# Kernel optimization log

Measured on AMD Instinct MI355X. Metric: run time of the kernel, lower is better.

Reference implementation:

```python
import jax, jax.numpy as jnp
from jax import lax
import numpy as np

T, B, H, L = 512, 64, 512, 2


def _ran_layer(x, c0, w_ih, w_hh, b, length):
    """x: [T,B,H], c0: [B,H]; returns (output [T,B,H], c_T [B,H])."""
    wi = jnp.einsum('tbi,ih->tbh', x, w_ih)  # precompute input projections

    def step(c, inp):
        t, x_t, wi_t = inp
        g = c @ w_hh + b + wi_t                      # [B, 2H]
        f, i = jnp.split(g, 2, axis=1)
        c1 = jax.nn.sigmoid(i) * x_t + jax.nn.sigmoid(f) * jnp.tanh(c)
        mask = (t < length)[:, None].astype(c1.dtype)  # length-mask blend
        c1 = c1 * mask + c * (1.0 - mask)
        return c1, c1

    ts = jnp.arange(x.shape[0])
    cT, out = lax.scan(step, c0, (ts, x, wi))
    return out, cT


def setup_inputs() -> dict:
    key = jax.random.key(0)
    ks = jax.random.split(key, 8)
    stdv = 1.0 / np.sqrt(H)

    def u(k, shape):
        return jax.random.uniform(k, shape, jnp.float32, -stdv, stdv)

    return {
        'input_': jax.random.normal(ks[0], (T, B, H), jnp.float32),
        'hx': jnp.zeros((L, B, H), jnp.float32),
        'length': jax.random.randint(ks[1], (B,), 0, T, jnp.int64 if jax.config.jax_enable_x64 else jnp.int32),
        'w_ih_0': u(ks[2], (H, 2 * H)),
        'w_hh_0': u(ks[3], (H, 2 * H)),
        'b_0': jnp.zeros((2 * H,), jnp.float32),
        'w_ih_1': u(ks[4], (H, 2 * H)),
        'w_hh_1': u(ks[5], (H, 2 * H)),
        'b_1': jnp.zeros((2 * H,), jnp.float32),
    }


def reference(input_, hx, length, w_ih_0, w_hh_0, b_0, w_ih_1, w_hh_1, b_1):
    params = [(w_ih_0, w_hh_0, b_0), (w_ih_1, w_hh_1, b_1)]
    x = input_
    c_n = []
    for layer in range(L):
        w_ih, w_hh, b = params[layer]
        x, cT = _ran_layer(x, hx[layer], w_ih, w_hh, b, length)
        c_n.append(cT)
    return x, jnp.stack(c_n, 0)
```

## Files before the change

kernel.cpp:

```cpp
#include <hip/hip_runtime.h>

#define T_ 512
#define B_ 64
#define H_ 512
#define G_ 1024

typedef _Float16 f16;
typedef _Float16 h2 __attribute__((ext_vector_type(2)));
typedef _Float16 h4 __attribute__((ext_vector_type(4)));
typedef _Float16 f16x8 __attribute__((ext_vector_type(8)));
typedef float f32x4 __attribute__((ext_vector_type(4)));
typedef unsigned long long u64;

#define SPINMAX (1 << 22)

__device__ __forceinline__ float dot8_h(uint4 w, uint4 c, float acc) {
    union U { uint4 u; h2 h[4]; };
    U uw; uw.u = w;
    U uc; uc.u = c;
#if defined(__has_builtin) && __has_builtin(__builtin_amdgcn_fdot2)
    acc = __builtin_amdgcn_fdot2(uw.h[0], uc.h[0], acc, false);
    acc = __builtin_amdgcn_fdot2(uw.h[1], uc.h[1], acc, false);
    acc = __builtin_amdgcn_fdot2(uw.h[2], uc.h[2], acc, false);
    acc = __builtin_amdgcn_fdot2(uw.h[3], uc.h[3], acc, false);
#else
#pragma unroll
    for (int i = 0; i < 4; ++i) {
        acc += (float)uw.h[i][0] * (float)uc.h[i][0];
        acc += (float)uw.h[i][1] * (float)uc.h[i][1];
    }
#endif
    return acc;
}

__device__ __forceinline__ float sigm(float x) { return 1.f / (1.f + __expf(-x)); }

__device__ __forceinline__ u64 ldA64(const u64* p) {
    return __hip_atomic_load(p, __ATOMIC_RELAXED, __HIP_MEMORY_SCOPE_AGENT);
}
__device__ __forceinline__ void stA32(unsigned* p, unsigned v) {
    __hip_atomic_store(p, v, __ATOMIC_RELAXED, __HIP_MEMORY_SCOPE_AGENT);
}

__global__ void pack_fp16(const float* __restrict__ src, uint4* __restrict__ dst) {
    int idx = blockIdx.x * 256 + threadIdx.x;
    int j  = idx & (G_ - 1);
    int k8 = idx >> 10;
    union U { uint4 u; f16 h[8]; } v;
#pragma unroll
    for (int i = 0; i < 8; ++i)
        v.h[i] = (f16)src[(size_t)(k8 * 8 + i) * G_ + j];
    dst[idx] = v.u;
}

__global__ void pack_wcols(const float* __restrict__ src, uint4* __restrict__ dst) {
    int idx = blockIdx.x * 256 + threadIdx.x;
    int col = idx & 1023, k2 = idx >> 10;
    union U { uint4 u; f16 h[8]; } v;
#pragma unroll
    for (int i = 0; i < 8; ++i)
        v.h[i] = (f16)src[(size_t)(k2 * 8 + i) * G_ + col];
    dst[(size_t)col * 64 + k2] = v.u;
}

__global__ void pack_wT(const float* __restrict__ w, f16* __restrict__ bt) {
    int idx = blockIdx.x * 256 + threadIdx.x;
    int k = idx & 511, n = idx >> 9;
    bt[idx] = (f16)w[(size_t)k * G_ + n];
}

__launch_bounds__(256, 2)
__global__ void mfma_gemm_axf32(const float* __restrict__ A, const f16* __restrict__ BT,
                                const float* __restrict__ bias, f16* __restrict__ C) {
    __shared__ __align__(16) f16 aLds[128][64 + 8];
    __shared__ __align__(16) f16 bLds[128][64 + 8];
    const int tid = threadIdx.x;
    const int bm = blockIdx.x, bn = blockIdx.y;
    const int lane = tid & 63, wid = tid >> 6;
    const int wm = wid & 1, wn = wid >> 1;
    const int fr = lane & 15, fg = lane >> 4;

    f32x4 acc[4][4] = {};

    for (int kt = 0; kt < 8; ++kt) {
#pragma unroll
        for (int p = 0; p < 8; ++p) {
            int i = p * 256 + tid;
            int row = i >> 4, kc = (i & 15) * 4;
            float4 av = *(const float4*)&A[((size_t)(bm * 128 + row)) * 512 + kt * 64 + kc];
            h4 hv = {(f16)av.x, (f16)av.y, (f16)av.z, (f16)av.w};
            *(h4*)&aLds[row][kc] = hv;
        }
#pragma unroll
        for (int p = 0; p < 4; ++p) {
            int i = p * 256 + tid;
            int row = i >> 3, slot = i & 7;
            uint4 bv = *(const uint4*)&BT[((size_t)(bn * 128 + row)) * 512 + kt * 64 + slot * 8];
            *(uint4*)&bLds[row][slot * 8] = bv;
        }
        __syncthreads();
#pragma unroll
        for (int kf = 0; kf < 2; ++kf) {
            const int k0 = kf * 32 + fg * 8;
            f16x8 af[4], bf[4];
#pragma unroll
            for (int mi = 0; mi < 4; ++mi)
                af[mi] = *(const f16x8*)&aLds[wm * 64 + mi * 16 + fr][k0];
#pragma unroll
            for (int ni = 0; ni < 4; ++ni)
                bf[ni] = *(const f16x8*)&bLds[wn * 64 + ni * 16 + fr][k0];
#pragma unroll
            for (int mi = 0; mi < 4; ++mi)
#pragma unroll
                for (int ni = 0; ni < 4; ++ni)
                    acc[mi][ni] = __builtin_amdgcn_mfma_f32_16x16x32_f16(
                        af[mi], bf[ni], acc[mi][ni], 0, 0, 0);
        }
        __syncthreads();
    }

#pragma unroll
    for (int mi = 0; mi < 4; ++mi) {
#pragma unroll
        for (int ni = 0; ni < 4; ++ni) {
            int n = bn * 128 + wn * 64 + ni * 16 + fr;
            float bv = bias[n];
#pragma unroll
            for (int r = 0; r < 4; ++r) {
                int m = bm * 128 + wm * 64 + mi * 16 + fg * 4 + r;
                C[(size_t)m * G_ + n] = (f16)(acc[mi][ni][r] + bv);
            }
        }
    }
}

#define GM 128
#define GN 64
#define GK 16
__launch_bounds__(256)
__global__ void gemm_bias_f16(const float* __restrict__ A,
                              const float* __restrict__ Bm,
                              const float* __restrict__ bias,
                              f16* __restrict__ C, int M) {
    __shared__ __align__(16) float Als[GK][GM + 4];
    __shared__ __align__(16) float Bls[GK][GN];
    int tid = threadIdx.x;
    int m_base = blockIdx.x * GM;
    int n_base = blockIdx.y * GN;
    int tx = tid & 15, ty = tid >> 4;
    int m0 = ty * 8, n0 = tx * 4;
    float acc[8][4] = {};

    for (int k0 = 0; k0 < H_; k0 += GK) {
#pragma unroll
        for (int r = 0; r < 2; ++r) {
            int idx2 = tid + 256 * r;
            int row = idx2 >> 2, kc = (idx2 & 3) * 4;
            float4 av = *(const float4*)&A[(size_t)(m_base + row) * H_ + k0 + kc];
            Als[kc + 0][row] = av.x;
            Als[kc + 1][row] = av.y;
            Als[kc + 2][row] = av.z;
            Als[kc + 3][row] = av.w;
        }
        {
            int kk = tid >> 4, colb = (tid & 15) * 4;
            float4 bv = *(const float4*)&Bm[(size_t)(k0 + kk) * G_ + n_base + colb];
            *(float4*)&Bls[kk][colb] = bv;
        }
        __syncthreads();
#pragma unroll
        for (int kk = 0; kk < GK; ++kk) {
            float a0[8], b0[4];
            *(float4*)&a0[0] = *(const float4*)&Als[kk][m0];
            *(float4*)&a0[4] = *(const float4*)&Als[kk][m0 + 4];
            *(float4*)&b0[0] = *(const float4*)&Bls[kk][n0];
#pragma unroll
            for (int im = 0; im < 8; ++im)
#pragma unroll
                for (int in = 0; in < 4; ++in)
                    acc[im][in] += a0[im] * b0[in];
        }
        __syncthreads();
    }
    float bv[4];
    *(float4*)&bv[0] = *(const float4*)&bias[n_base + n0];
#pragma unroll
    for (int im = 0; im < 8; ++im) {
        h4 hv;
#pragma unroll
        for (int in = 0; in < 4; ++in) hv[in] = (f16)(acc[im][in] + bv[in]);
        *(h4*)&C[(size_t)(m_base + m0 + im) * G_ + n_base + n0] = hv;
    }
}

template <int PATH>
__launch_bounds__(1024, 1)
__global__ void ran_scan(const float* __restrict__ x_in, float* __restrict__ x_out,
                         float* __restrict__ c_out, const float* __restrict__ c0,
                         const int* __restrict__ length,
                         const uint4* __restrict__ whh_p,
                         const f16* __restrict__ wi, const float* __restrict__ bias,
                         const float* __restrict__ whh_f, const float* __restrict__ wih_f) {
    __shared__ __align__(16) f16 c_h[H_];
    __shared__ __align__(16) float c_f32[H_];
    __shared__ __align__(16) float x_f32[H_];
    __shared__ float g_i_lds[H_];

    const int b = blockIdx.x, tid = threadIdx.x;
    int len = length[b];
    if (len < 0) len = 0;
    if (len > T_) len = T_;

    float c1 = 0.f;
    if (tid < H_) {
        c1 = c0[(size_t)b * H_ + tid];
        c_h[tid] = (f16)c1;
        if (PATH == 2) c_f32[tid] = c1;
    }
    const float bj = (PATH == 0) ? 0.f : bias[tid];
    __syncthreads();

    for (int t = 0; t < len; ++t) {
        const size_t base = ((size_t)t * B_ + b) * H_;
        float xv = 0.f;
        if (tid < H_) {
            xv = x_in[base + tid];
            if (PATH == 2) x_f32[tid] = xv;
        }
        if (PATH == 2) __syncthreads();

        float g;
        if (PATH == 0) g = (float)wi[((size_t)t * B_ + b) * G_ + tid];
        else           g = bj;

        if (PATH == 0) {
            const uint4* cc = (const uint4*)c_h;
#pragma unroll 4
            for (int k8 = 0; k8 < H_ / 8; ++k8)
                g = dot8_h(whh_p[(size_t)k8 * G_ + tid], cc[k8], g);
        } else {
#pragma unroll 2
            for (int k = 0; k < H_; k += 4) {
                float4 cv = *(const float4*)&c_f32[k];
                g += cv.x * whh_f[(size_t)(k + 0) * G_ + tid];
                g += cv.y * whh_f[(size_t)(k + 1) * G_ + tid];
                g += cv.z * whh_f[(size_t)(k + 2) * G_ + tid];
                g += cv.w * whh_f[(size_t)(k + 3) * G_ + tid];
            }
#pragma unroll 2
            for (int k = 0; k < H_; k += 4) {
                float4 xvv = *(const float4*)&x_f32[k];
                g += xvv.x * wih_f[(size_t)(k + 0) * G_ + tid];
                g += xvv.y * wih_f[(size_t)(k + 1) * G_ + tid];
                g += xvv.z * wih_f[(size_t)(k + 2) * G_ + tid];
                g += xvv.w * wih_f[(size_t)(k + 3) * G_ + tid];
            }
        }

        if (tid >= H_) g_i_lds[tid - H_] = g;
        __syncthreads();
        if (tid < H_) {
            float gi = g_i_lds[tid];
            float c_old = c1;
            c1 = sigm(gi) * xv + sigm(g) * tanhf(c_old);
            c_h[tid] = (f16)c1;
            if (PATH == 2) c_f32[tid] = c1;
            x_out[base + tid] = c1;
        }
        __syncthreads();
    }

    if (tid < H_) {
        for (int t = len; t < T_; ++t)
            x_out[((size_t)t * B_ + b) * H_ + tid] = c1;
        c_out[(size_t)b * H_ + tid] = c1;
    }
}

__global__ __launch_bounds__(1024, 1)
void scan_mfma16(const float* __restrict__ x_in, const f16* __restrict__ wi,
                 const uint4* __restrict__ wpack, const float* __restrict__ c0,
                 const int* __restrict__ length, float* __restrict__ out,
                 float* __restrict__ cn, unsigned* __restrict__ cbuf,
                 int base_tag) {
    __shared__ __align__(16) f16 c_h[2][H_];
    __shared__ __align__(16) float2 g_part[2][128];
    __shared__ float c_fin[2][64];

    const int tid = threadIdx.x;
    const int bg = blockIdx.x & 31, s = blockIdx.x >> 5;
    const int b0 = bg * 2;
    const int w = tid >> 6, lane = tid & 63;
    const int n16 = lane & 15, kg = lane >> 4;
    const int p_grp = w >> 1, h = w & 1;

    const int gc = p_grp * 16 + n16;
    const int gcol = (gc < 64) ? (s * 64 + gc) : (512 + s * 64 + (gc - 64));
    uint4 wreg[8];
    {
        const uint4* wp = wpack + (size_t)gcol * 64 + kg;
#pragma unroll
        for (int k = 0; k < 8; ++k) wreg[k] = wp[(h * 8 + k) * 4];
    }

    if (tid < H_) {
        c_h[0][tid] = (f16)c0[(size_t)b0 * H_ + tid];
        c_h[1][tid] = (f16)c0[(size_t)(b0 + 1) * H_ + tid];
    }
    int len0 = length[b0], len1 = length[b0 + 1];
    len0 = min(max(len0, 0), T_);
    len1 = min(max(len1, 0), T_);
    const int maxlen = max(len0, len1);

    const int ab = (n16 < 2) ? n16 : 1;
    const int fb = tid >> 6, fcol = tid & 63;
    const int jj = s * 64 + fcol;
    const int myb = b0 + fb;
    const int mylen = fb ? len1 : len0;
    float c_old = 0.f;
    if (tid < 128) c_old = c0[(size_t)myb * H_ + jj];
    __syncthreads();

    for (int t = 0; t < maxlen; ++t) {
        float xv = 0.f, wif = 0.f, wii = 0.f;
        if (tid < 128) {
            size_t rb = (size_t)t * B_ + myb;
            xv  = x_in[rb * H_ + jj];
            wif = (float)wi[rb * G_ + jj];
            wii = (float)wi[rb * G_ + 512 + jj];
        }

        {
            f32x4 acc = {};
#pragma unroll
            for (int k = 0; k < 8; ++k) {
                const int m = h * 8 + k;
                f16x8 af = *(const f16x8*)&c_h[ab][m * 32 + kg * 8];
                acc = __builtin_amdgcn_mfma_f32_16x16x32_f16(
                    af, *(const f16x8*)&wreg[k], acc, 0, 0, 0);
            }
            if (lane < 16)
                g_part[h][p_grp * 16 + lane] = make_float2(acc[0], acc[1]);
        }
        __syncthreads();

        const int p1 = (t + 1) & 1;
        const unsigned tagw = (unsigned)(base_tag + t + 1) & 0xffffu;

        if (tid < 128) {
            float2 vf0 = g_part[0][fcol],      vf1 = g_part[1][fcol];
            float2 vi0 = g_part[0][64 + fcol], vi1 = g_part[1][64 + fcol];
            float gf = (fb ? (vf0.y + vf1.y) : (vf0.x + vf1.x)) + wif;
            float gi = (fb ? (vi0.y + vi1.y) : (vi0.x + vi1.x)) + wii;
            float c1;
            if (t < mylen) {
                float e2 = __expf(2.f * c_old);
                float th = (e2 - 1.f) / (e2 + 1.f);
                c1 = sigm(gi) * xv + sigm(gf) * th;
            } else {
                c1 = c_old;
            }
            c_old = c1;
            union { f16 h2u; unsigned short u; } cv;
            cv.h2u = (f16)c1;
            stA32(&cbuf[((size_t)(p1 * B_ + myb) << 9) + jj],
                  (tagw << 16) | (unsigned)cv.u);
            out[((size_t)t * B_ + myb) * H_ + jj] = c1;
            c_h[fb][jj] = cv.h2u;
        }

        if (t + 1 < maxlen && tid < 512) {
            int bidx = tid >> 8;
            int e = (tid & 255) * 2;
            if ((unsigned)(e - s * 64) >= 64u) {
                const u64 want2 = ((u64)tagw << 48) | ((u64)tagw << 16);
                const u64 mask2 = 0xffff0000ffff0000ull;
                const u64* pb = (const u64*)(cbuf +
                                   ((size_t)(p1 * B_ + b0 + bidx) << 9) + e);
                u64 v = ldA64(pb);
                int gd = 0;
                while ((v & mask2) != want2) {
                    if (++gd > SPINMAX) break;
                    if (gd > 16) __builtin_amdgcn_s_sleep(2);
                    v = ldA64(pb);
                }
                unsigned lo = (unsigned)v & 0xffffu;
                unsigned hi = (unsigned)(v >> 32) & 0xffffu;
                *(unsigned*)&c_h[bidx][e] = lo | (hi << 16);
            }
        }
        __syncthreads();
    }

    if (tid < 128) {
        c_fin[fb][fcol] = c_old;
        cn[(size_t)myb * H_ + jj] = c_old;
    }
    __syncthreads();

    const int ntail = T_ - maxlen;
    for (int i = tid; i < ntail * 128; i += 1024) {
        int tb = i >> 7;
        int cc = i & 127;
        int tfb = cc >> 6, tfc = cc & 63;
        out[((size_t)(maxlen + tb) * B_ + b0 + tfb) * H_ + s * 64 + tfc] =
            c_fin[tfb][tfc];
    }
}

extern "C" void kernel_launch(void* const* d_in, const int* in_sizes, int n_in,
                              void* d_out, int out_size, void* d_ws, size_t ws_size,
                              hipStream_t stream) {
    const float* input_ = (const float*)d_in[0];
    const float* hx     = (const float*)d_in[1];
    const int*   length = (const int*)d_in[2];
    const float* w_ih_0 = (const float*)d_in[3];
    const float* w_hh_0 = (const float*)d_in[4];
    const float* b_0    = (const float*)d_in[5];
    const float* w_ih_1 = (const float*)d_in[6];
    const float* w_hh_1 = (const float*)d_in[7];
    const float* b_1    = (const float*)d_in[8];

    float* out = (float*)d_out;
    float* cn  = out + (size_t)T_ * B_ * H_;

    char* wsb = (char*)d_ws;
    const size_t MB = 1u << 20;
    const size_t WI_BYTES = (size_t)T_ * B_ * G_ * sizeof(f16);
    const int M = T_ * B_;

    const size_t need1 = WI_BYTES + 2 * MB + 256 * 1024;
    const size_t needA = 2 * MB + WI_BYTES;

    if (ws_size >= need1) {
        f16*      wi    = (f16*)wsb;
        uint4*    wpack = (uint4*)(wsb + WI_BYTES);
        f16*      bt    = (f16*)(wsb + WI_BYTES + MB);
        unsigned* cbuf  = (unsigned*)(wsb + WI_BYTES + 2 * MB);

        hipMemsetAsync(cbuf, 0, 256 * 1024, stream);

        pack_wcols<<<256, 256, 0, stream>>>(w_hh_0, wpack);
        pack_wT<<<2048, 256, 0, stream>>>(w_ih_0, bt);
        mfma_gemm_axf32<<<dim3(M / 128, G_ / 128), 256, 0, stream>>>(input_, bt, b_0, wi);
        scan_mfma16<<<256, 1024, 0, stream>>>(input_, wi, wpack, hx, length,
                                              out, cn, cbuf, 0);
        pack_wcols<<<256, 256, 0, stream>>>(w_hh_1, wpack);
        pack_wT<<<2048, 256, 0, stream>>>(w_ih_1, bt);
        mfma_gemm_axf32<<<dim3(M / 128, G_ / 128), 256, 0, stream>>>(out, bt, b_1, wi);
        scan_mfma16<<<256, 1024, 0, stream>>>(out, wi, wpack,
                                              hx + (size_t)B_ * H_, length,
                                              out, cn + (size_t)B_ * H_, cbuf, T_);
    } else if (ws_size >= needA) {
        uint4* whh0 = (uint4*)(wsb + 0 * MB);
        uint4* whh1 = (uint4*)(wsb + 1 * MB);
        f16* wi = (f16*)(wsb + 2 * MB);
        pack_fp16<<<256, 256, 0, stream>>>(w_hh_0, whh0);
        pack_fp16<<<256, 256, 0, stream>>>(w_hh_1, whh1);

        gemm_bias_f16<<<dim3(M / GM, G_ / GN), 256, 0, stream>>>(input_, w_ih_0, b_0, wi, M);
        ran_scan<0><<<64, 1024, 0, stream>>>(input_, out, cn, hx, length,
                                             whh0, wi, b_0, nullptr, nullptr);
        gemm_bias_f16<<<dim3(M / GM, G_ / GN), 256, 0, stream>>>(out, w_ih_1, b_1, wi, M);
        ran_scan<0><<<64, 1024, 0, stream>>>(out, out, cn + (size_t)B_ * H_,
                                             hx + (size_t)B_ * H_, length,
                                             whh1, wi, b_1, nullptr, nullptr);
    } else {
        ran_scan<2><<<64, 1024, 0, stream>>>(input_, out, cn, hx, length,
                                             nullptr, nullptr, b_0, w_hh_0, w_ih_0);
        ran_scan<2><<<64, 1024, 0, stream>>>(out, out, cn + (size_t)B_ * H_,
                                             hx + (size_t)B_ * H_, length,
                                             nullptr, nullptr, b_1, w_hh_1, w_ih_1);
    }
}
```

Measured before the change: 1.684 ms.

## Halve scan block to 512 threads with full-K MFMA per wave

The recurrent scan kernel now runs with 512 threads per block instead of 1024. Each wave keeps all 16 K-chunks of its weight column slice in registers and computes the full dot product itself, using two accumulators, rather than splitting K across wave pairs. This drops the cross-wave partial-sum reduction and shrinks the per-step block barrier to fewer waves. In exchange it doubles the weight registers per thread and the serial MFMA chain length per wave, which lengthens each step's critical path.

```diff
diff --git a/kernel.cpp b/kernel.cpp
--- a/kernel.cpp
+++ b/kernel.cpp
@@ -277,14 +277,14 @@
     }
 }
 
-__global__ __launch_bounds__(1024, 1)
-void scan_mfma16(const float* __restrict__ x_in, const f16* __restrict__ wi,
-                 const uint4* __restrict__ wpack, const float* __restrict__ c0,
-                 const int* __restrict__ length, float* __restrict__ out,
-                 float* __restrict__ cn, unsigned* __restrict__ cbuf,
-                 int base_tag) {
+__global__ __launch_bounds__(512, 1)
+void scan_mfma(const float* __restrict__ x_in, const f16* __restrict__ wi,
+               const uint4* __restrict__ wpack, const float* __restrict__ c0,
+               const int* __restrict__ length, float* __restrict__ out,
+               float* __restrict__ cn, unsigned* __restrict__ cbuf,
+               int base_tag) {
     __shared__ __align__(16) f16 c_h[2][H_];
-    __shared__ __align__(16) float2 g_part[2][128];
+    __shared__ __align__(16) float2 g_buf[128];
     __shared__ float c_fin[2][64];
 
     const int tid = threadIdx.x;
@@ -292,20 +292,21 @@
     const int b0 = bg * 2;
     const int w = tid >> 6, lane = tid & 63;
     const int n16 = lane & 15, kg = lane >> 4;
-    const int p_grp = w >> 1, h = w & 1;
-
-    const int gc = p_grp * 16 + n16;
+
+    const int gc = w * 16 + n16;
     const int gcol = (gc < 64) ? (s * 64 + gc) : (512 + s * 64 + (gc - 64));
-    uint4 wreg[8];
+    uint4 wreg[16];
     {
         const uint4* wp = wpack + (size_t)gcol * 64 + kg;
 #pragma unroll
-        for (int k = 0; k < 8; ++k) wreg[k] = wp[(h * 8 + k) * 4];
-    }
-
-    if (tid < H_) {
-        c_h[0][tid] = (f16)c0[(size_t)b0 * H_ + tid];
-        c_h[1][tid] = (f16)c0[(size_t)(b0 + 1) * H_ + tid];
+        for (int m = 0; m < 16; ++m) wreg[m] = wp[m * 4];
+    }
+
+    {
+        float a = c0[(size_t)b0 * H_ + tid];
+        float b = c0[(size_t)(b0 + 1) * H_ + tid];
+        c_h[0][tid] = (f16)a;
+        c_h[1][tid] = (f16)b;
     }
     int len0 = length[b0], len1 = length[b0 + 1];
     len0 = min(max(len0, 0), T_);
@@ -331,16 +332,22 @@
         }
 
         {
-            f32x4 acc = {};
-#pragma unroll
-            for (int k = 0; k < 8; ++k) {
-                const int m = h * 8 + k;
+            f32x4 acc0 = {}, acc1 = {};
+#pragma unroll
+            for (int m = 0; m < 8; ++m) {
                 f16x8 af = *(const f16x8*)&c_h[ab][m * 32 + kg * 8];
-                acc = __builtin_amdgcn_mfma_f32_16x16x32_f16(
-                    af, *(const f16x8*)&wreg[k], acc, 0, 0, 0);
+                acc0 = __builtin_amdgcn_mfma_f32_16x16x32_f16(
+                    af, *(const f16x8*)&wreg[m], acc0, 0, 0, 0);
+            }
+#pragma unroll
+            for (int m = 8; m < 16; ++m) {
+                f16x8 af = *(const f16x8*)&c_h[ab][m * 32 + kg * 8];
+                acc1 = __builtin_amdgcn_mfma_f32_16x16x32_f16(
+                    af, *(const f16x8*)&wreg[m], acc1, 0, 0, 0);
             }
             if (lane < 16)
-                g_part[h][p_grp * 16 + lane] = make_float2(acc[0], acc[1]);
+                g_buf[w * 16 + lane] =
+                    make_float2(acc0[0] + acc1[0], acc0[1] + acc1[1]);
         }
         __syncthreads();
 
@@ -348,10 +355,10 @@
         const unsigned tagw = (unsigned)(base_tag + t + 1) & 0xffffu;
 
         if (tid < 128) {
-            float2 vf0 = g_part[0][fcol],      vf1 = g_part[1][fcol];
-            float2 vi0 = g_part[0][64 + fcol], vi1 = g_part[1][64 + fcol];
-            float gf = (fb ? (vf0.y + vf1.y) : (vf0.x + vf1.x)) + wif;
-            float gi = (fb ? (vi0.y + vi1.y) : (vi0.x + vi1.x)) + wii;
+            float2 vf = g_buf[fcol];
+            float2 vi = g_buf[64 + fcol];
+            float gf = (fb ? vf.y : vf.x) + wif;
+            float gi = (fb ? vi.y : vi.x) + wii;
             float c1;
             if (t < mylen) {
                 float e2 = __expf(2.f * c_old);
@@ -361,15 +368,15 @@
                 c1 = c_old;
             }
             c_old = c1;
-            union { f16 h2u; unsigned short u; } cv;
-            cv.h2u = (f16)c1;
+            union { f16 h; unsigned short u; } cv;
+            cv.h = (f16)c1;
             stA32(&cbuf[((size_t)(p1 * B_ + myb) << 9) + jj],
                   (tagw << 16) | (unsigned)cv.u);
             out[((size_t)t * B_ + myb) * H_ + jj] = c1;
-            c_h[fb][jj] = cv.h2u;
-        }
-
-        if (t + 1 < maxlen && tid < 512) {
+            c_h[fb][jj] = cv.h;
+        }
+
+        if (t + 1 < maxlen) {
             int bidx = tid >> 8;
             int e = (tid & 255) * 2;
             if ((unsigned)(e - s * 64) >= 64u) {
@@ -399,7 +406,7 @@
     __syncthreads();
 
     const int ntail = T_ - maxlen;
-    for (int i = tid; i < ntail * 128; i += 1024) {
+    for (int i = tid; i < ntail * 128; i += 512) {
         int tb = i >> 7;
         int cc = i & 127;
         int tfb = cc >> 6, tfc = cc & 63;
@@ -443,14 +450,14 @@
         pack_wcols<<<256, 256, 0, stream>>>(w_hh_0, wpack);
         pack_wT<<<2048, 256, 0, stream>>>(w_ih_0, bt);
         mfma_gemm_axf32<<<dim3(M / 128, G_ / 128), 256, 0, stream>>>(input_, bt, b_0, wi);
-        scan_mfma16<<<256, 1024, 0, stream>>>(input_, wi, wpack, hx, length,
-                                              out, cn, cbuf, 0);
+        scan_mfma<<<256, 512, 0, stream>>>(input_, wi, wpack, hx, length,
+                                           out, cn, cbuf, 0);
         pack_wcols<<<256, 256, 0, stream>>>(w_hh_1, wpack);
         pack_wT<<<2048, 256, 0, stream>>>(w_ih_1, bt);
         mfma_gemm_axf32<<<dim3(M / 128, G_ / 128), 256, 0, stream>>>(out, bt, b_1, wi);
-        scan_mfma16<<<256, 1024, 0, stream>>>(out, wi, wpack,
-                                              hx + (size_t)B_ * H_, length,
-                                              out, cn + (size_t)B_ * H_, cbuf, T_);
+        scan_mfma<<<256, 512, 0, stream>>>(out, wi, wpack,
+                                           hx + (size_t)B_ * H_, length,
+                                           out, cn + (size_t)B_ * H_, cbuf, T_);
     } else if (ws_size >= needA) {
         uint4* whh0 = (uint4*)(wsb + 0 * MB);
         uint4* whh1 = (uint4*)(wsb + 1 * MB);
```

Measured after the change: 1.673 ms. About the same (-0.6%).
